# Performance work log

Measured on AMD Instinct MI355X. Metric: run time of the kernel, lower is better.

Reference implementation:

```python
import jax, jax.numpy as jnp
import numpy as np

V = 20000   # input_size (POI vocab)
U = 10000   # user_count
H = 128     # hidden_size
B = 64      # user_len (batch)
S = 200     # seq_len
LAM_T = 0.01
LAM_S = 100.0
DAY = 86400.0


def setup_inputs() -> dict:
    key = jax.random.key(0)
    ks = jax.random.split(key, 12)
    sc = 1.0 / np.sqrt(H)
    return {
        "poi_inputs": jax.random.randint(ks[0], (B, S), 0, V),
        "lengths": jnp.full((B,), S, dtype=jnp.int32),  # full sequences -> pack/pad is identity
        "timestamp_inputs": jnp.sort(jax.random.uniform(ks[1], (B, S), minval=0.0, maxval=DAY), axis=1),
        "location_inputs": jax.random.normal(ks[2], (B, S, 2)) * 0.1,
        "active_user": jax.random.randint(ks[3], (B,), 0, U),
        "emb_W": jax.random.normal(ks[4], (V, H)),      # nn.Embedding default N(0,1)
        "user_W": jax.random.normal(ks[5], (U, H)),
        "W_ih": jax.random.uniform(ks[6], (H, H), minval=-sc, maxval=sc),
        "W_hh": jax.random.uniform(ks[7], (H, H), minval=-sc, maxval=sc),
        "b_ih": jax.random.uniform(ks[8], (H,), minval=-sc, maxval=sc),
        "b_hh": jax.random.uniform(ks[9], (H,), minval=-sc, maxval=sc),
        "fc_W": jax.random.uniform(ks[10], (V, 2 * H), minval=-sc, maxval=sc),  # torch Linear [out,in]
        "fc_b": jax.random.uniform(ks[11], (V,), minval=-sc, maxval=sc),
    }


def _safe_norm(d):
    # norm over last axis with zero (not nan) gradient at d == 0
    d2 = jnp.sum(d * d, axis=-1)
    pos = d2 > 0
    return jnp.where(pos, jnp.sqrt(jnp.where(pos, d2, 1.0)), 0.0)


def reference(poi_inputs, lengths, timestamp_inputs, location_inputs, active_user,
              emb_W, user_W, W_ih, W_hh, b_ih, b_hh, fc_W, fc_b):
    t, s = timestamp_inputs, location_inputs
    x_emb = emb_W[poi_inputs]                       # [B,S,H]

    # vanilla tanh RNN (torch nn.RNN, batch_first) via scan over time
    def step(h, xt):
        h = jnp.tanh(xt @ W_ih.T + b_ih + h @ W_hh.T + b_hh)
        return h, h
    h0 = jnp.zeros((x_emb.shape[0], W_hh.shape[0]), x_emb.dtype)
    _, out = jax.lax.scan(step, h0, jnp.swapaxes(x_emb, 0, 1))
    out = jnp.swapaxes(out, 0, 1)                   # [B,S,H]

    # vectorized spatio-temporal decay attention (original O(S^2) python loop)
    dt = jnp.maximum(t[:, :, None] - t[:, None, :], 0.0)          # [B,S,S] clamp_min(0)
    ds = _safe_norm(s[:, :, None, :] - s[:, None, :, :])          # [B,S,S]
    a_j = ((jnp.cos(dt * (2.0 * jnp.pi / DAY)) + 1.0) * 0.5) * jnp.exp(-dt * LAM_T)
    b_j = jnp.exp(-ds * LAM_S)
    causal = jnp.tril(jnp.ones((t.shape[1], t.shape[1]), bool))   # j <= i
    w = jnp.where(causal, a_j * b_j + 1e-10, 0.0)                 # [B,S,S]
    sum_w = jnp.maximum(jnp.sum(w, axis=-1), 1e-10)               # [B,S]
    out_w = jnp.einsum('bij,bjh->bih', w, out) / sum_w[..., None] # [B,S,H]

    p_u = jnp.broadcast_to(user_W[active_user][:, None, :], out_w.shape)
    out_pu = jnp.concatenate([out_w, p_u], axis=-1)               # [B,S,2H]
    y = jax.nn.softmax(out_pu @ fc_W.T + fc_b, axis=-1)           # [B,S,V]
    return y, out_pu
```

## Files before the change

### kernel.cpp

```cpp
#include <hip/hip_runtime.h>
#include <hip/hip_bf16.h>
#include <stdint.h>

#define B_   64
#define S_   200
#define H_   128
#define V_   20000
#define M_   12800
#define NPAD 20224
#define NBN  158
#define NBM  100
#define NWG2 15800

#define WS_A      0u
#define WS_FCW    3276800u
#define WS_U      8454144u
#define WS_RSUM   13631488u
#define WS_WTIH   13682688u

#define XP_OFF    0
#define HOUT_OFF  2000000
#define PART_OFF  4000000
#define OUTPU_OFF 256000000ll

typedef __attribute__((ext_vector_type(8))) __bf16 bf16x8;
typedef __attribute__((ext_vector_type(4))) float  f32x4;

__device__ __forceinline__ void gll16(const void* g, void* l) {
  __builtin_amdgcn_global_load_lds(
      (const __attribute__((address_space(1))) void*)g,
      (__attribute__((address_space(3))) void*)l, 16, 0, 0);
}

__global__ __launch_bounds__(128)
void prep_wt(const float* __restrict__ w_ih, float* __restrict__ wt) {
  int bid = blockIdx.x, t = threadIdx.x;
  wt[bid * 128 + t] = w_ih[t * 128 + bid];
}

__global__ __launch_bounds__(128)
void xproj_k(const int* __restrict__ poi, const float* __restrict__ emb,
             const float* __restrict__ wt_ih, const float* __restrict__ b_ih,
             const float* __restrict__ b_hh, float* __restrict__ xp) {
  __shared__ float xs[16][128];
  int j = threadIdx.x;
  int m0 = blockIdx.x * 16;
#pragma unroll
  for (int i = 0; i < 16; ++i)
    xs[i][j] = emb[(long)poi[m0 + i] * 128 + j];
  __syncthreads();
  float bias = b_ih[j] + b_hh[j];
  float acc[16];
#pragma unroll
  for (int i = 0; i < 16; ++i) acc[i] = bias;
  for (int kq = 0; kq < 32; ++kq) {
    float w0 = wt_ih[(4 * kq + 0) * 128 + j];
    float w1 = wt_ih[(4 * kq + 1) * 128 + j];
    float w2 = wt_ih[(4 * kq + 2) * 128 + j];
    float w3 = wt_ih[(4 * kq + 3) * 128 + j];
#pragma unroll
    for (int i = 0; i < 16; ++i) {
      float4 xv = *(const float4*)&xs[i][4 * kq];
      acc[i] = fmaf(xv.x, w0, acc[i]);
      acc[i] = fmaf(xv.y, w1, acc[i]);
      acc[i] = fmaf(xv.z, w2, acc[i]);
      acc[i] = fmaf(xv.w, w3, acc[i]);
    }
  }
#pragma unroll
  for (int i = 0; i < 16; ++i)
    xp[(long)(m0 + i) * 128 + j] = acc[i];
}

__global__ __launch_bounds__(256)
void fused_pre(const float* __restrict__ xp, const float* __restrict__ w_hh,
               float* __restrict__ hout,
               const float* __restrict__ fcW, __hip_bfloat16* __restrict__ w1,
               const int* __restrict__ auser, const float* __restrict__ userW,
               const float* __restrict__ fcb, float* __restrict__ U) {
  __shared__ float smem_u[8][128];
  int blk = blockIdx.x;
  int t = threadIdx.x;

  if (blk < 64) {
    int b = blk, j = t & 127;
    float* hs = (float*)smem_u;
    float w[128];
#pragma unroll
    for (int k = 0; k < 128; ++k) w[k] = w_hh[j * 128 + k];
    hs[j] = 0.f;
    __syncthreads();
    int cur = 0;
    for (int tt = 0; tt < S_; ++tt) {
      float x0 = xp[((long)b * S_ + tt) * 128 + j];
      const float4* hp4 = (const float4*)(hs + cur * 128);
      float a0 = 0.f, a1 = 0.f, a2 = 0.f, a3 = 0.f;
#pragma unroll
      for (int k = 0; k < 8; ++k) {
        float4 v0 = hp4[k], v1 = hp4[k + 8], v2 = hp4[k + 16], v3 = hp4[k + 24];
        a0 = fmaf(v0.x, w[4 * k + 0], a0); a0 = fmaf(v0.y, w[4 * k + 1], a0);
        a0 = fmaf(v0.z, w[4 * k + 2], a0); a0 = fmaf(v0.w, w[4 * k + 3], a0);
        a1 = fmaf(v1.x, w[32 + 4 * k + 0], a1); a1 = fmaf(v1.y, w[32 + 4 * k + 1], a1);
        a1 = fmaf(v1.z, w[32 + 4 * k + 2], a1); a1 = fmaf(v1.w, w[32 + 4 * k + 3], a1);
        a2 = fmaf(v2.x, w[64 + 4 * k + 0], a2); a2 = fmaf(v2.y, w[64 + 4 * k + 1], a2);
        a2 = fmaf(v2.z, w[64 + 4 * k + 2], a2); a2 = fmaf(v2.w, w[64 + 4 * k + 3], a2);
        a3 = fmaf(v3.x, w[96 + 4 * k + 0], a3); a3 = fmaf(v3.y, w[96 + 4 * k + 1], a3);
        a3 = fmaf(v3.z, w[96 + 4 * k + 2], a3); a3 = fmaf(v3.w, w[96 + 4 * k + 3], a3);
      }
      float hn = tanhf(x0 + ((a0 + a1) + (a2 + a3)));
      hs[(cur ^ 1) * 128 + j] = hn;
      hout[((long)b * S_ + tt) * 128 + j] = hn;
      cur ^= 1;
      __syncthreads();
    }
  } else if (blk < 222) {
    int row = (blk - 64) * 128 + (t >> 1);
    int c0 = (t & 1) * 64;
    const float* src = fcW + (long)row * 256 + c0;
    __hip_bfloat16* dst = w1 + (long)row * 128 + c0;
    bool valid = row < V_;
#pragma unroll
    for (int q = 0; q < 8; ++q) {
      float4 v0, v1;
      if (valid) { v0 = *(const float4*)(src + q * 8); v1 = *(const float4*)(src + q * 8 + 4); }
      else { v0 = make_float4(0.f, 0.f, 0.f, 0.f); v1 = v0; }
      ushort4 p0, p1;
      p0.x = __bfloat16_as_ushort(__float2bfloat16(v0.x));
      p0.y = __bfloat16_as_ushort(__float2bfloat16(v0.y));
      p0.z = __bfloat16_as_ushort(__float2bfloat16(v0.z));
      p0.w = __bfloat16_as_ushort(__float2bfloat16(v0.w));
      p1.x = __bfloat16_as_ushort(__float2bfloat16(v1.x));
      p1.y = __bfloat16_as_ushort(__float2bfloat16(v1.y));
      p1.z = __bfloat16_as_ushort(__float2bfloat16(v1.z));
      p1.w = __bfloat16_as_ushort(__float2bfloat16(v1.w));
      *(ushort4*)(dst + q * 8)     = p0;
      *(ushort4*)(dst + q * 8 + 4) = p1;
    }
  } else {
    int idx = blk - 222;
    int cb = idx % 79, bgrp = idx / 79;
    int c = cb * 256 + t;
    int b0 = bgrp * 8;
    for (int i = t; i < 8 * 128; i += 256) {
      int bb = i >> 7, kk = i & 127;
      smem_u[bb][kk] = userW[(long)auser[b0 + bb] * 128 + kk];
    }
    __syncthreads();
    float acc[8];
#pragma unroll
    for (int bb = 0; bb < 8; ++bb) acc[bb] = 0.f;
    if (c < V_) {
      const float* w2 = fcW + (long)c * 256 + 128;
      for (int kq = 0; kq < 32; ++kq) {
        float4 wv = *(const float4*)(w2 + 4 * kq);
#pragma unroll
        for (int bb = 0; bb < 8; ++bb) {
          float4 uv = *(const float4*)&smem_u[bb][4 * kq];
          acc[bb] = fmaf(wv.x, uv.x, acc[bb]);
          acc[bb] = fmaf(wv.y, uv.y, acc[bb]);
          acc[bb] = fmaf(wv.z, uv.z, acc[bb]);
          acc[bb] = fmaf(wv.w, uv.w, acc[bb]);
        }
      }
      float base = fcb[c];
#pragma unroll
      for (int bb = 0; bb < 8; ++bb)
        U[(long)(b0 + bb) * NPAD + c] = base + acc[bb];
    } else {
#pragma unroll
      for (int bb = 0; bb < 8; ++bb)
        U[(long)(b0 + bb) * NPAD + c] = -1e30f;
    }
  }
}

__global__ __launch_bounds__(128)
void attn_k(const float* __restrict__ ts, const float* __restrict__ loc,
            const float* __restrict__ hout, const int* __restrict__ auser,
            const float* __restrict__ userW, float* __restrict__ outpu,
            __hip_bfloat16* __restrict__ Abf) {
  int i = blockIdx.x, b = blockIdx.y, h = threadIdx.x;
  __shared__ float wl[128];
  const float OMEGA = 7.27220521664304e-05f;
  float ti = ts[b * S_ + i];
  float lx = loc[(b * S_ + i) * 2 + 0];
  float ly = loc[(b * S_ + i) * 2 + 1];
  float acc = 0.f, sw = 0.f;
  for (int jc = 0; jc <= i; jc += 128) {
    int j = jc + h;
    float wj = 0.f;
    if (j <= i) {
      float dt = fmaxf(ti - ts[b * S_ + j], 0.f);
      float a = (cosf(dt * OMEGA) + 1.f) * 0.5f * expf(-dt * 0.01f);
      float dx = lx - loc[(b * S_ + j) * 2 + 0];
      float dy = ly - loc[(b * S_ + j) * 2 + 1];
      float dn = sqrtf(dx * dx + dy * dy);
      wj = a * expf(-dn * 100.f) + 1e-10f;
    }
    __syncthreads();
    wl[h] = wj;
    __syncthreads();
    int lim = min(128, i - jc + 1);
    const float* hb = hout + ((long)b * S_ + jc) * 128 + h;
    int jj = 0;
    for (; jj + 4 <= lim; jj += 4) {
      float4 wv4 = *(const float4*)&wl[jj];
      float h0 = hb[(long)(jj + 0) * 128];
      float h1 = hb[(long)(jj + 1) * 128];
      float h2 = hb[(long)(jj + 2) * 128];
      float h3 = hb[(long)(jj + 3) * 128];
      acc = fmaf(wv4.x, h0, acc); sw += wv4.x;
      acc = fmaf(wv4.y, h1, acc); sw += wv4.y;
      acc = fmaf(wv4.z, h2, acc); sw += wv4.z;
      acc = fmaf(wv4.w, h3, acc); sw += wv4.w;
    }
    for (; jj < lim; ++jj) {
      float wv = wl[jj];
      acc = fmaf(wv, hb[(long)jj * 128], acc);
      sw += wv;
    }
  }
  float ow = acc / fmaxf(sw, 1e-10f);
  long m = (long)b * S_ + i;
  float pu = userW[(long)auser[b] * 128 + h];
  outpu[m * 256 + h]       = ow;
  outpu[m * 256 + 128 + h] = pu;
  Abf[m * 128 + h]         = __float2bfloat16(ow);
}

template <int PASS>
__global__ __launch_bounds__(512, 4)
void gemm_fc(const __hip_bfloat16* __restrict__ A,
             const __hip_bfloat16* __restrict__ Bw,
             const float* __restrict__ Ut,
             const float* __restrict__ rowsum,
             float* __restrict__ part,
             float* __restrict__ y) {
  __shared__ __align__(16) char smem[65536];
  __shared__ float rsum4[4][128];
  char* AsB = smem;
  char* BsB = smem + 32768;
  float* lbuf = (float*)smem;

  const int tid  = threadIdx.x;
  const int lane = tid & 63;
  const int wid  = tid >> 6;
  const int wr = wid >> 2, wc = wid & 3;
  const int g = lane >> 4, lr = lane & 15;

  const int orig = blockIdx.x;
  const int nid = (orig & 7) * (NWG2 / 8) + (orig >> 3);
  const int bn = nid / NBM, bm = nid % NBM;
  const long brow = (long)bm * 128, bcol = (long)bn * 128;

  const char* Ab = (const char*)A + brow * 256;
  const char* Bb = (const char*)Bw + bcol * 256;

#pragma unroll
  for (int i = 0; i < 4; ++i) {
    int ci = i * 512 + tid;
    int row = ci >> 4;
    int w = (ci & 15) ^ (row & 7);
    long src = (long)row * 256 + (long)w * 16;
    gll16(Ab + src, AsB + (long)ci * 16);
    gll16(Bb + src, BsB + (long)ci * 16);
  }
  __syncthreads();

  f32x4 acc[4][2];
#pragma unroll
  for (int mi = 0; mi < 4; ++mi)
#pragma unroll
    for (int ni = 0; ni < 2; ++ni) acc[mi][ni] = (f32x4)(0.f);

#pragma unroll
  for (int kk = 0; kk < 4; ++kk) {
    bf16x8 af[4], bfr[2];
#pragma unroll
    for (int mi = 0; mi < 4; ++mi) {
      int row = wr * 64 + mi * 16 + lr;
      int w = ((kk << 2) | g) ^ (row & 7);
      af[mi] = *(const bf16x8*)(AsB + row * 256 + w * 16);
    }
#pragma unroll
    for (int ni = 0; ni < 2; ++ni) {
      int row = wc * 32 + ni * 16 + lr;
      int w = ((kk << 2) | g) ^ (row & 7);
      bfr[ni] = *(const bf16x8*)(BsB + row * 256 + w * 16);
    }
#pragma unroll
    for (int mi = 0; mi < 4; ++mi)
#pragma unroll
      for (int ni = 0; ni < 2; ++ni)
        acc[mi][ni] = __builtin_amdgcn_mfma_f32_16x16x32_bf16(af[mi], bfr[ni], acc[mi][ni], 0, 0, 0);
  }

  if (PASS == 0) {
#pragma unroll
    for (int mi = 0; mi < 4; ++mi) {
#pragma unroll
      for (int r = 0; r < 4; ++r) {
        long row = brow + wr * 64 + mi * 16 + g * 4 + r;
        const float* urow = Ut + (long)(row / S_) * NPAD + bcol;
        float s = 0.f;
#pragma unroll
        for (int ni = 0; ni < 2; ++ni) {
          float u = urow[wc * 32 + ni * 16 + lr];
          s += __expf(acc[mi][ni][r] + u);
        }
#pragma unroll
        for (int off = 1; off < 16; off <<= 1) s += __shfl_xor(s, off);
        if (lr == 0) rsum4[wc][wr * 64 + mi * 16 + g * 4 + r] = s;
      }
    }
    __syncthreads();
    if (tid < 128)
      part[(long)bn * M_ + brow + tid] =
          rsum4[0][tid] + rsum4[1][tid] + rsum4[2][tid] + rsum4[3][tid];
  } else {
    if (bcol >= V_) return;
    const bool full = (bcol + 128 <= V_);
    __syncthreads();
#pragma unroll
    for (int mi = 0; mi < 4; ++mi) {
#pragma unroll
      for (int r = 0; r < 4; ++r) {
        int lrow = wr * 64 + mi * 16 + g * 4 + r;
        long row = brow + lrow;
        const float* urow = Ut + (long)(row / S_) * NPAD + bcol;
        float inv = 1.0f / rowsum[row];
        int key = ((lrow >> 2) & 3) << 2;
#pragma unroll
        for (int ni = 0; ni < 2; ++ni) {
          int lcol = wc * 32 + ni * 16 + lr;
          lbuf[lrow * 128 + (lcol ^ key)] = __expf(acc[mi][ni][r] + urow[lcol]) * inv;
        }
      }
    }
    __syncthreads();
    if (full) {
#pragma unroll
      for (int it = 0; it < 8; ++it) {
        int idx = it * 512 + tid;
        int lrow = idx >> 5, c4 = idx & 31;
        int key = ((lrow >> 2) & 3) << 2;
        f32x4 v = *(const f32x4*)(lbuf + lrow * 128 + ((c4 * 4) ^ key));
        __builtin_nontemporal_store(v,
            (f32x4*)(y + (brow + lrow) * (long)V_ + bcol + c4 * 4));
      }
    } else {
#pragma unroll
      for (int it = 0; it < 8; ++it) {
        int idx = it * 512 + tid;
        int lrow = idx >> 5, c4 = idx & 31;
        int key = ((lrow >> 2) & 3) << 2;
        const float* src = lbuf + lrow * 128 + ((c4 * 4) ^ key);
        long row = brow + lrow;
#pragma unroll
        for (int e = 0; e < 4; ++e) {
          int col = (int)bcol + c4 * 4 + e;
          if (col < V_) y[row * (long)V_ + col] = src[e];
        }
      }
    }
  }
}

__global__ void reduce_rows(const float* __restrict__ part, float* __restrict__ rowsum) {
  int m = blockIdx.x * 256 + threadIdx.x;
  if (m < M_) {
    float s = 0.f;
    for (int bn = 0; bn < NBN; ++bn) s += part[(long)bn * M_ + m];
    rowsum[m] = fmaxf(s, 1e-30f);
  }
}

extern "C" void kernel_launch(void* const* d_in, const int* in_sizes, int n_in,
                              void* d_out, int out_size, void* d_ws, size_t ws_size,
                              hipStream_t stream) {
  const int*   poi   = (const int*)d_in[0];
  const float* ts    = (const float*)d_in[2];
  const float* loc   = (const float*)d_in[3];
  const int*   auser = (const int*)d_in[4];
  const float* embW  = (const float*)d_in[5];
  const float* userW = (const float*)d_in[6];
  const float* w_ih  = (const float*)d_in[7];
  const float* w_hh  = (const float*)d_in[8];
  const float* b_ih  = (const float*)d_in[9];
  const float* b_hh  = (const float*)d_in[10];
  const float* fcW   = (const float*)d_in[11];
  const float* fcb   = (const float*)d_in[12];

  float* out = (float*)d_out;
  char*  ws  = (char*)d_ws;
  __hip_bfloat16* Abf    = (__hip_bfloat16*)(ws + WS_A);
  __hip_bfloat16* w1b    = (__hip_bfloat16*)(ws + WS_FCW);
  float*          Ut     = (float*)(ws + WS_U);
  float*          rowsum = (float*)(ws + WS_RSUM);
  float*          wt_ih  = (float*)(ws + WS_WTIH);

  float* xp    = out + XP_OFF;
  float* hout  = out + HOUT_OFF;
  float* part  = out + PART_OFF;
  float* outpu = out + OUTPU_OFF;

  prep_wt<<<dim3(128), dim3(128), 0, stream>>>(w_ih, wt_ih);
  xproj_k<<<dim3(M_ / 16), dim3(128), 0, stream>>>(poi, embW, wt_ih, b_ih, b_hh, xp);
  fused_pre<<<dim3(64 + 158 + 632), dim3(256), 0, stream>>>(
      xp, w_hh, hout, fcW, w1b, auser, userW, fcb, Ut);
  attn_k<<<dim3(S_, B_), dim3(128), 0, stream>>>(ts, loc, hout, auser, userW, outpu, Abf);
  gemm_fc<0><<<dim3(NWG2), dim3(512), 0, stream>>>(Abf, w1b, Ut, nullptr, part, nullptr);
  reduce_rows<<<dim3(50), dim3(256), 0, stream>>>(part, rowsum);
  gemm_fc<1><<<dim3(NWG2), dim3(512), 0, stream>>>(Abf, w1b, Ut, rowsum, nullptr, out);
}
```

Baseline: 734.7 us.

## Make FC GEMM persistent with A-tile reuse and double-buffered B prefetch

New measurement: 949.5 us. 1.29x slower.

```diff
diff --git a/kernel.cpp b/kernel.cpp
--- a/kernel.cpp
+++ b/kernel.cpp
@@ -11,6 +11,7 @@
 #define NBN  158
 #define NBM  100
 #define NWG2 15800
+#define PBLK 256
 
 #define WS_A      0u
 #define WS_FCW    3276800u
@@ -229,18 +230,17 @@
 }
 
 template <int PASS>
-__global__ __launch_bounds__(512, 4)
-void gemm_fc(const __hip_bfloat16* __restrict__ A,
-             const __hip_bfloat16* __restrict__ Bw,
-             const float* __restrict__ Ut,
-             const float* __restrict__ rowsum,
-             float* __restrict__ part,
-             float* __restrict__ y) {
-  __shared__ __align__(16) char smem[65536];
-  __shared__ float rsum4[4][128];
-  char* AsB = smem;
-  char* BsB = smem + 32768;
-  float* lbuf = (float*)smem;
+__global__ __launch_bounds__(512, 2)
+void gemm_p(const __hip_bfloat16* __restrict__ A,
+            const __hip_bfloat16* __restrict__ Bw,
+            const float* __restrict__ Ut,
+            const float* __restrict__ rowsum,
+            float* __restrict__ part,
+            float* __restrict__ y) {
+  __shared__ __align__(16) char As[32768];
+  __shared__ __align__(16) char Bs[2][32768];
+  __shared__ __align__(16) char Ls[32768];
+  float* Lf = (float*)Ls;
 
   const int tid  = threadIdx.x;
   const int lane = tid & 63;
@@ -248,121 +248,158 @@
   const int wr = wid >> 2, wc = wid & 3;
   const int g = lane >> 4, lr = lane & 15;
 
-  const int orig = blockIdx.x;
-  const int nid = (orig & 7) * (NWG2 / 8) + (orig >> 3);
-  const int bn = nid / NBM, bm = nid % NBM;
-  const long brow = (long)bm * 128, bcol = (long)bn * 128;
-
-  const char* Ab = (const char*)A + brow * 256;
-  const char* Bb = (const char*)Bw + bcol * 256;
-
-#pragma unroll
-  for (int i = 0; i < 4; ++i) {
-    int ci = i * 512 + tid;
-    int row = ci >> 4;
-    int w = (ci & 15) ^ (row & 7);
-    long src = (long)row * 256 + (long)w * 16;
-    gll16(Ab + src, AsB + (long)ci * 16);
-    gll16(Bb + src, BsB + (long)ci * 16);
-  }
-  __syncthreads();
-
-  f32x4 acc[4][2];
-#pragma unroll
-  for (int mi = 0; mi < 4; ++mi)
-#pragma unroll
-    for (int ni = 0; ni < 2; ++ni) acc[mi][ni] = (f32x4)(0.f);
-
-#pragma unroll
-  for (int kk = 0; kk < 4; ++kk) {
-    bf16x8 af[4], bfr[2];
-#pragma unroll
-    for (int mi = 0; mi < 4; ++mi) {
-      int row = wr * 64 + mi * 16 + lr;
-      int w = ((kk << 2) | g) ^ (row & 7);
-      af[mi] = *(const bf16x8*)(AsB + row * 256 + w * 16);
-    }
-#pragma unroll
-    for (int ni = 0; ni < 2; ++ni) {
-      int row = wc * 32 + ni * 16 + lr;
-      int w = ((kk << 2) | g) ^ (row & 7);
-      bfr[ni] = *(const bf16x8*)(BsB + row * 256 + w * 16);
-    }
+  const int blk = blockIdx.x;
+  const int tB = (NWG2 * blk) / PBLK;
+  const int tE = (NWG2 * (blk + 1)) / PBLK;
+
+  int curbm = -1;
+  int buf = 0;
+
+  for (int t = tB; t < tE; ++t) {
+    const int bm = t / NBN;
+    const int bn = t - bm * NBN;
+    const long brow = (long)bm * 128;
+    const long bcol = (long)bn * 128;
+
+    if (bm != curbm) {
+      const char* Ab = (const char*)A + brow * 256;
+      const char* Bb = (const char*)Bw + bcol * 256;
+#pragma unroll
+      for (int i = 0; i < 4; ++i) {
+        int ci = i * 512 + tid;
+        int row = ci >> 4;
+        int w = (ci & 15) ^ (row & 7);
+        gll16(Ab + (long)row * 256 + w * 16, As + (long)ci * 16);
+        gll16(Bb + (long)row * 256 + w * 16, Bs[buf] + (long)ci * 16);
+      }
+      asm volatile("s_waitcnt vmcnt(0)" ::: "memory");
+      __builtin_amdgcn_s_barrier();
+      curbm = bm;
+    }
+
+    const bool pf = (t + 1 < tE) && ((t + 1) / NBN == bm);
+    if (pf) {
+      const char* Bb = (const char*)Bw + (bcol + 128) * 256;
+#pragma unroll
+      for (int i = 0; i < 4; ++i) {
+        int ci = i * 512 + tid;
+        int row = ci >> 4;
+        int w = (ci & 15) ^ (row & 7);
+        gll16(Bb + (long)row * 256 + w * 16, Bs[buf ^ 1] + (long)ci * 16);
+      }
+    }
+
+    f32x4 acc[4][2];
 #pragma unroll
     for (int mi = 0; mi < 4; ++mi)
 #pragma unroll
-      for (int ni = 0; ni < 2; ++ni)
-        acc[mi][ni] = __builtin_amdgcn_mfma_f32_16x16x32_bf16(af[mi], bfr[ni], acc[mi][ni], 0, 0, 0);
-  }
-
-  if (PASS == 0) {
-#pragma unroll
-    for (int mi = 0; mi < 4; ++mi) {
-#pragma unroll
-      for (int r = 0; r < 4; ++r) {
-        long row = brow + wr * 64 + mi * 16 + g * 4 + r;
-        const float* urow = Ut + (long)(row / S_) * NPAD + bcol;
-        float s = 0.f;
-#pragma unroll
-        for (int ni = 0; ni < 2; ++ni) {
-          float u = urow[wc * 32 + ni * 16 + lr];
-          s += __expf(acc[mi][ni][r] + u);
+      for (int ni = 0; ni < 2; ++ni) acc[mi][ni] = (f32x4)(0.f);
+    const char* Bcur = Bs[buf];
+#pragma unroll
+    for (int kk = 0; kk < 4; ++kk) {
+      bf16x8 af[4], bfr[2];
+#pragma unroll
+      for (int mi = 0; mi < 4; ++mi) {
+        int row = wr * 64 + mi * 16 + lr;
+        int w = ((kk << 2) | g) ^ (row & 7);
+        af[mi] = *(const bf16x8*)(As + row * 256 + w * 16);
+      }
+#pragma unroll
+      for (int ni = 0; ni < 2; ++ni) {
+        int row = wc * 32 + ni * 16 + lr;
+        int w = ((kk << 2) | g) ^ (row & 7);
+        bfr[ni] = *(const bf16x8*)(Bcur + row * 256 + w * 16);
+      }
+#pragma unroll
+      for (int mi = 0; mi < 4; ++mi)
+#pragma unroll
+        for (int ni = 0; ni < 2; ++ni)
+          acc[mi][ni] = __builtin_amdgcn_mfma_f32_16x16x32_bf16(af[mi], bfr[ni], acc[mi][ni], 0, 0, 0);
+    }
+
+    if (PASS == 0) {
+#pragma unroll
+      for (int mi = 0; mi < 4; ++mi) {
+#pragma unroll
+        for (int r = 0; r < 4; ++r) {
+          long row = brow + wr * 64 + mi * 16 + g * 4 + r;
+          const float* urow = Ut + (long)(row / S_) * NPAD + bcol;
+          float s = 0.f;
+#pragma unroll
+          for (int ni = 0; ni < 2; ++ni) {
+            float u = urow[wc * 32 + ni * 16 + lr];
+            s += __expf(acc[mi][ni][r] + u);
+          }
+#pragma unroll
+          for (int off = 1; off < 16; off <<= 1) s += __shfl_xor(s, off);
+          if (lr == 0) Lf[wc * 128 + wr * 64 + mi * 16 + g * 4 + r] = s;
         }
-#pragma unroll
-        for (int off = 1; off < 16; off <<= 1) s += __shfl_xor(s, off);
-        if (lr == 0) rsum4[wc][wr * 64 + mi * 16 + g * 4 + r] = s;
-      }
-    }
-    __syncthreads();
-    if (tid < 128)
-      part[(long)bn * M_ + brow + tid] =
-          rsum4[0][tid] + rsum4[1][tid] + rsum4[2][tid] + rsum4[3][tid];
-  } else {
-    if (bcol >= V_) return;
-    const bool full = (bcol + 128 <= V_);
-    __syncthreads();
-#pragma unroll
-    for (int mi = 0; mi < 4; ++mi) {
-#pragma unroll
-      for (int r = 0; r < 4; ++r) {
-        int lrow = wr * 64 + mi * 16 + g * 4 + r;
-        long row = brow + lrow;
-        const float* urow = Ut + (long)(row / S_) * NPAD + bcol;
-        float inv = 1.0f / rowsum[row];
-        int key = ((lrow >> 2) & 3) << 2;
-#pragma unroll
-        for (int ni = 0; ni < 2; ++ni) {
-          int lcol = wc * 32 + ni * 16 + lr;
-          lbuf[lrow * 128 + (lcol ^ key)] = __expf(acc[mi][ni][r] + urow[lcol]) * inv;
+      }
+      asm volatile("s_waitcnt lgkmcnt(0)" ::: "memory");
+      __builtin_amdgcn_s_barrier();
+      if (tid < 128)
+        part[(long)bn * M_ + brow + tid] =
+            Lf[tid] + Lf[128 + tid] + Lf[256 + tid] + Lf[384 + tid];
+      asm volatile("" ::: "memory");
+    } else {
+      if (bn < 157) {
+        const bool full = (bn < 156);
+#pragma unroll
+        for (int half = 0; half < 2; ++half) {
+          if (wr == half) {
+#pragma unroll
+            for (int mi = 0; mi < 4; ++mi) {
+#pragma unroll
+              for (int r = 0; r < 4; ++r) {
+                int lrow = mi * 16 + g * 4 + r;
+                long row = brow + half * 64 + lrow;
+                const float* urow = Ut + (long)(row / S_) * NPAD + bcol;
+                float inv = 1.0f / rowsum[row];
+                int key = ((lrow >> 2) & 3) << 2;
+#pragma unroll
+                for (int ni = 0; ni < 2; ++ni) {
+                  int lcol = wc * 32 + ni * 16 + lr;
+                  Lf[lrow * 128 + (lcol ^ key)] = __expf(acc[mi][ni][r] + urow[lcol]) * inv;
+                }
+              }
+            }
+          }
+          asm volatile("s_waitcnt lgkmcnt(0)" ::: "memory");
+          __builtin_amdgcn_s_barrier();
+#pragma unroll
+          for (int it = 0; it < 4; ++it) {
+            int idx = it * 512 + tid;
+            int lrow = idx >> 5, c4 = idx & 31;
+            int key = ((lrow >> 2) & 3) << 2;
+            long row = brow + half * 64 + lrow;
+            if (full) {
+              f32x4 v = *(const f32x4*)(Lf + lrow * 128 + ((c4 * 4) ^ key));
+              __builtin_nontemporal_store(v,
+                  (f32x4*)(y + row * (long)V_ + bcol + c4 * 4));
+            } else {
+              const float* srcp = Lf + lrow * 128 + ((c4 * 4) ^ key);
+#pragma unroll
+              for (int e = 0; e < 4; ++e) {
+                int col = (int)bcol + c4 * 4 + e;
+                if (col < V_) y[row * (long)V_ + col] = srcp[e];
+              }
+            }
+          }
+          asm volatile("" ::: "memory");
+          __builtin_amdgcn_s_barrier();
         }
       }
     }
-    __syncthreads();
-    if (full) {
-#pragma unroll
-      for (int it = 0; it < 8; ++it) {
-        int idx = it * 512 + tid;
-        int lrow = idx >> 5, c4 = idx & 31;
-        int key = ((lrow >> 2) & 3) << 2;
-        f32x4 v = *(const f32x4*)(lbuf + lrow * 128 + ((c4 * 4) ^ key));
-        __builtin_nontemporal_store(v,
-            (f32x4*)(y + (brow + lrow) * (long)V_ + bcol + c4 * 4));
-      }
+
+    if (pf) {
+      if (PASS == 0)            asm volatile("s_waitcnt vmcnt(1)" ::: "memory");
+      else if (bn < 156)        asm volatile("s_waitcnt vmcnt(8)" ::: "memory");
+      else                      asm volatile("s_waitcnt vmcnt(0)" ::: "memory");
     } else {
-#pragma unroll
-      for (int it = 0; it < 8; ++it) {
-        int idx = it * 512 + tid;
-        int lrow = idx >> 5, c4 = idx & 31;
-        int key = ((lrow >> 2) & 3) << 2;
-        const float* src = lbuf + lrow * 128 + ((c4 * 4) ^ key);
-        long row = brow + lrow;
-#pragma unroll
-        for (int e = 0; e < 4; ++e) {
-          int col = (int)bcol + c4 * 4 + e;
-          if (col < V_) y[row * (long)V_ + col] = src[e];
-        }
-      }
-    }
+      asm volatile("s_waitcnt vmcnt(0)" ::: "memory");
+    }
+    __builtin_amdgcn_s_barrier();
+    buf ^= 1;
   }
 }
 
@@ -409,7 +446,7 @@
   fused_pre<<<dim3(64 + 158 + 632), dim3(256), 0, stream>>>(
       xp, w_hh, hout, fcW, w1b, auser, userW, fcb, Ut);
   attn_k<<<dim3(S_, B_), dim3(128), 0, stream>>>(ts, loc, hout, auser, userW, outpu, Abf);
-  gemm_fc<0><<<dim3(NWG2), dim3(512), 0, stream>>>(Abf, w1b, Ut, nullptr, part, nullptr);
+  gemm_p<0><<<dim3(PBLK), dim3(512), 0, stream>>>(Abf, w1b, Ut, nullptr, part, nullptr);
   reduce_rows<<<dim3(50), dim3(256), 0, stream>>>(part, rowsum);
-  gemm_fc<1><<<dim3(NWG2), dim3(512), 0, stream>>>(Abf, w1b, Ut, rowsum, nullptr, out);
-}
+  gemm_p<1><<<dim3(PBLK), dim3(512), 0, stream>>>(Abf, w1b, Ut, rowsum, nullptr, out);
+}
```

## Load GEMM fragments directly from global memory with smaller 64-row tiles

Applied to the files above, without the earlier changes.

Result: slower. 1.089 ms (+48.2%).

```diff
diff --git a/kernel.cpp b/kernel.cpp
--- a/kernel.cpp
+++ b/kernel.cpp
@@ -9,8 +9,8 @@
 #define M_   12800
 #define NPAD 20224
 #define NBN  158
-#define NBM  100
-#define NWG2 15800
+#define NBMD 200
+#define NWGD 31600
 
 #define WS_A      0u
 #define WS_FCW    3276800u
@@ -25,12 +25,6 @@
 
 typedef __attribute__((ext_vector_type(8))) __bf16 bf16x8;
 typedef __attribute__((ext_vector_type(4))) float  f32x4;
-
-__device__ __forceinline__ void gll16(const void* g, void* l) {
-  __builtin_amdgcn_global_load_lds(
-      (const __attribute__((address_space(1))) void*)g,
-      (__attribute__((address_space(3))) void*)l, 16, 0, 0);
-}
 
 __global__ __launch_bounds__(128)
 void prep_wt(const float* __restrict__ w_ih, float* __restrict__ wt) {
@@ -229,44 +223,28 @@
 }
 
 template <int PASS>
-__global__ __launch_bounds__(512, 4)
-void gemm_fc(const __hip_bfloat16* __restrict__ A,
-             const __hip_bfloat16* __restrict__ Bw,
-             const float* __restrict__ Ut,
-             const float* __restrict__ rowsum,
-             float* __restrict__ part,
-             float* __restrict__ y) {
-  __shared__ __align__(16) char smem[65536];
-  __shared__ float rsum4[4][128];
-  char* AsB = smem;
-  char* BsB = smem + 32768;
-  float* lbuf = (float*)smem;
+__global__ __launch_bounds__(256, 5)
+void gemm_d(const __hip_bfloat16* __restrict__ A,
+            const __hip_bfloat16* __restrict__ Bw,
+            const float* __restrict__ Ut,
+            const float* __restrict__ rowsum,
+            float* __restrict__ part,
+            float* __restrict__ y) {
+  __shared__ __align__(16) float Lf[64 * 128];
 
   const int tid  = threadIdx.x;
   const int lane = tid & 63;
-  const int wid  = tid >> 6;
-  const int wr = wid >> 2, wc = wid & 3;
+  const int wc   = tid >> 6;
   const int g = lane >> 4, lr = lane & 15;
 
   const int orig = blockIdx.x;
-  const int nid = (orig & 7) * (NWG2 / 8) + (orig >> 3);
-  const int bn = nid / NBM, bm = nid % NBM;
-  const long brow = (long)bm * 128, bcol = (long)bn * 128;
+  const int nid = (orig & 7) * (NWGD / 8) + (orig >> 3);
+  const int bn = nid / NBMD, bm = nid % NBMD;
+  const long brow = (long)bm * 64, bcol = (long)bn * 128;
 
   const char* Ab = (const char*)A + brow * 256;
   const char* Bb = (const char*)Bw + bcol * 256;
 
-#pragma unroll
-  for (int i = 0; i < 4; ++i) {
-    int ci = i * 512 + tid;
-    int row = ci >> 4;
-    int w = (ci & 15) ^ (row & 7);
-    long src = (long)row * 256 + (long)w * 16;
-    gll16(Ab + src, AsB + (long)ci * 16);
-    gll16(Bb + src, BsB + (long)ci * 16);
-  }
-  __syncthreads();
-
   f32x4 acc[4][2];
 #pragma unroll
   for (int mi = 0; mi < 4; ++mi)
@@ -277,17 +255,11 @@
   for (int kk = 0; kk < 4; ++kk) {
     bf16x8 af[4], bfr[2];
 #pragma unroll
-    for (int mi = 0; mi < 4; ++mi) {
-      int row = wr * 64 + mi * 16 + lr;
-      int w = ((kk << 2) | g) ^ (row & 7);
-      af[mi] = *(const bf16x8*)(AsB + row * 256 + w * 16);
-    }
-#pragma unroll
-    for (int ni = 0; ni < 2; ++ni) {
-      int row = wc * 32 + ni * 16 + lr;
-      int w = ((kk << 2) | g) ^ (row & 7);
-      bfr[ni] = *(const bf16x8*)(BsB + row * 256 + w * 16);
-    }
+    for (int mi = 0; mi < 4; ++mi)
+      af[mi] = *(const bf16x8*)(Ab + (long)(mi * 16 + lr) * 256 + (kk * 4 + g) * 16);
+#pragma unroll
+    for (int ni = 0; ni < 2; ++ni)
+      bfr[ni] = *(const bf16x8*)(Bb + (long)(wc * 32 + ni * 16 + lr) * 256 + (kk * 4 + g) * 16);
 #pragma unroll
     for (int mi = 0; mi < 4; ++mi)
 #pragma unroll
@@ -300,7 +272,7 @@
     for (int mi = 0; mi < 4; ++mi) {
 #pragma unroll
       for (int r = 0; r < 4; ++r) {
-        long row = brow + wr * 64 + mi * 16 + g * 4 + r;
+        long row = brow + mi * 16 + g * 4 + r;
         const float* urow = Ut + (long)(row / S_) * NPAD + bcol;
         float s = 0.f;
 #pragma unroll
@@ -310,22 +282,21 @@
         }
 #pragma unroll
         for (int off = 1; off < 16; off <<= 1) s += __shfl_xor(s, off);
-        if (lr == 0) rsum4[wc][wr * 64 + mi * 16 + g * 4 + r] = s;
-      }
-    }
-    __syncthreads();
-    if (tid < 128)
+        if (lr == 0) Lf[wc * 64 + mi * 16 + g * 4 + r] = s;
+      }
+    }
+    __syncthreads();
+    if (tid < 64)
       part[(long)bn * M_ + brow + tid] =
-          rsum4[0][tid] + rsum4[1][tid] + rsum4[2][tid] + rsum4[3][tid];
+          Lf[tid] + Lf[64 + tid] + Lf[128 + tid] + Lf[192 + tid];
   } else {
     if (bcol >= V_) return;
     const bool full = (bcol + 128 <= V_);
-    __syncthreads();
 #pragma unroll
     for (int mi = 0; mi < 4; ++mi) {
 #pragma unroll
       for (int r = 0; r < 4; ++r) {
-        int lrow = wr * 64 + mi * 16 + g * 4 + r;
+        int lrow = mi * 16 + g * 4 + r;
         long row = brow + lrow;
         const float* urow = Ut + (long)(row / S_) * NPAD + bcol;
         float inv = 1.0f / rowsum[row];
@@ -333,7 +304,7 @@
 #pragma unroll
         for (int ni = 0; ni < 2; ++ni) {
           int lcol = wc * 32 + ni * 16 + lr;
-          lbuf[lrow * 128 + (lcol ^ key)] = __expf(acc[mi][ni][r] + urow[lcol]) * inv;
+          Lf[lrow * 128 + (lcol ^ key)] = __expf(acc[mi][ni][r] + urow[lcol]) * inv;
         }
       }
     }
@@ -341,20 +312,20 @@
     if (full) {
 #pragma unroll
       for (int it = 0; it < 8; ++it) {
-        int idx = it * 512 + tid;
+        int idx = it * 256 + tid;
         int lrow = idx >> 5, c4 = idx & 31;
         int key = ((lrow >> 2) & 3) << 2;
-        f32x4 v = *(const f32x4*)(lbuf + lrow * 128 + ((c4 * 4) ^ key));
+        f32x4 v = *(const f32x4*)(Lf + lrow * 128 + ((c4 * 4) ^ key));
         __builtin_nontemporal_store(v,
             (f32x4*)(y + (brow + lrow) * (long)V_ + bcol + c4 * 4));
       }
     } else {
 #pragma unroll
       for (int it = 0; it < 8; ++it) {
-        int idx = it * 512 + tid;
+        int idx = it * 256 + tid;
         int lrow = idx >> 5, c4 = idx & 31;
         int key = ((lrow >> 2) & 3) << 2;
-        const float* src = lbuf + lrow * 128 + ((c4 * 4) ^ key);
+        const float* src = Lf + lrow * 128 + ((c4 * 4) ^ key);
         long row = brow + lrow;
 #pragma unroll
         for (int e = 0; e < 4; ++e) {
@@ -409,7 +380,7 @@
   fused_pre<<<dim3(64 + 158 + 632), dim3(256), 0, stream>>>(
       xp, w_hh, hout, fcW, w1b, auser, userW, fcb, Ut);
   attn_k<<<dim3(S_, B_), dim3(128), 0, stream>>>(ts, loc, hout, auser, userW, outpu, Abf);
-  gemm_fc<0><<<dim3(NWG2), dim3(512), 0, stream>>>(Abf, w1b, Ut, nullptr, part, nullptr);
+  gemm_d<0><<<dim3(NWGD), dim3(256), 0, stream>>>(Abf, w1b, Ut, nullptr, part, nullptr);
   reduce_rows<<<dim3(50), dim3(256), 0, stream>>>(part, rowsum);
-  gemm_fc<1><<<dim3(NWG2), dim3(512), 0, stream>>>(Abf, w1b, Ut, rowsum, nullptr, out);
-}
+  gemm_d<1><<<dim3(NWGD), dim3(256), 0, stream>>>(Abf, w1b, Ut, rowsum, nullptr, out);
+}
```
